# Optimization experiments

Hardware: AMD Instinct MI355X
Metric: run time of the kernel (lower is better)

Reference implementation:

```python
import jax, jax.numpy as jnp
import numpy as np


def setup_inputs() -> dict:
    key = jax.random.key(0)
    ks = jax.random.split(key, 5)
    B, S, D, U = 16, 4096, 256, 256
    scale = 1.0 / np.sqrt(D)
    return {
        "values": jax.random.normal(ks[0], (B, S, D), dtype=jnp.float32),
        "query": jax.random.normal(ks[1], (B, D), dtype=jnp.float32),
        "W1": jax.random.normal(ks[2], (D, U), dtype=jnp.float32) * scale,
        "b1": jnp.zeros((U,), dtype=jnp.float32),
        "W2": jax.random.normal(ks[3], (D, U), dtype=jnp.float32) * scale,
        "b2": jnp.zeros((U,), dtype=jnp.float32),
        "V": jax.random.normal(ks[4], (U, 1), dtype=jnp.float32) * (1.0 / np.sqrt(U)),
        "bV": jnp.zeros((1,), dtype=jnp.float32),
    }


def reference(values, query, W1, b1, W2, b2, V, bV):
    # values: [B, S, D], query: [B, D]
    proj_v = jnp.einsum("bsd,du->bsu", values, W1) + b1          # [B, S, U]
    proj_q = (query @ W2 + b2)[:, None, :]                        # [B, 1, U]
    score = jnp.tanh(proj_v + proj_q) @ V + bV                    # [B, S, 1]
    attention_weights = jax.nn.softmax(score, axis=1)             # [B, S, 1]
    context_vector = jnp.sum(attention_weights * values, axis=1)  # [B, D]
    return context_vector, attention_weights
```

## Files before the change

kernel.cpp:

```cpp
#include <hip/hip_runtime.h>
#include <hip/hip_bf16.h>

#define B 16
#define S 4096
#define D 256
#define U 256
#define ROWS 64
#define CHUNK 128
#define NCH (S / CHUNK)

typedef short short8 __attribute__((ext_vector_type(8)));
typedef float f32x4 __attribute__((ext_vector_type(4)));

__device__ __forceinline__ ushort f2bf(float f) {
    union { float f; uint u; } x{f};
    uint r = (x.u + 0x7fffu + ((x.u >> 16) & 1u)) >> 16;
    return (ushort)r;
}

__device__ __forceinline__ float fast_tanh(float x) {
    float e = __expf(2.0f * x);
    return 1.0f - 2.0f * __builtin_amdgcn_rcpf(e + 1.0f);
}

__global__ void ka_setup(const float* __restrict__ q, const float* __restrict__ W2,
                         const float* __restrict__ b2, const float* __restrict__ b1,
                         const float* __restrict__ W1, float* __restrict__ pqb,
                         ushort* __restrict__ W1p, float* __restrict__ ctx) {
    int bid = blockIdx.x, t = threadIdx.x;
    if (bid < 16) {
        int b = bid, u = t;
        const float* qb = q + b * D;
        float acc = b2[u] + b1[u];
#pragma unroll 8
        for (int d = 0; d < D; ++d)
            acc = fmaf(qb[d], W2[d * U + u], acc);
        pqb[b * U + u] = acc;
    } else if (bid < 24) {
        int kk = bid - 16;
        int l = t & 63, g = t >> 6;
        int colu0 = l & 15;
        int k0 = kk * 32 + (l >> 4) * 8;
#pragma unroll
        for (int i = 0; i < 4; ++i) {
            int nt = g * 4 + i;
            int colu = nt * 16 + colu0;
            ushort* dst = W1p + (((nt * 8) + kk) * 64 + l) * 8;
#pragma unroll
            for (int e = 0; e < 8; ++e) dst[e] = f2bf(W1[(k0 + e) * U + colu]);
        }
    } else {
        int i = (bid - 24) * 256 + t;
        ctx[i] = 0.f;
        ctx[i + 2048] = 0.f;
    }
}

__global__ void kb_scores(const float* __restrict__ values, const ushort* __restrict__ W1p,
                          const float* __restrict__ pqb, const float* __restrict__ V,
                          const float* __restrict__ bV, float* __restrict__ scores,
                          float* __restrict__ cstats) {
    __shared__ ushort Alds[ROWS * 256];
    __shared__ float red[4][ROWS];
    int b = blockIdx.x >> 6;
    int s0 = (blockIdx.x & 63) * ROWS;
    int t = threadIdx.x;
    int w = t >> 6, l = t & 63;
    char* lds = (char*)Alds;

    const float* src = values + ((size_t)(b * S + s0)) * D;
#pragma unroll
    for (int i = 0; i < 16; ++i) {
        int row = i * 4 + w;
        int col = l * 4;
        float4 v = *(const float4*)&src[row * 256 + col];
        ushort4 h;
        h.x = f2bf(v.x); h.y = f2bf(v.y); h.z = f2bf(v.z); h.w = f2bf(v.w);
        int byte = (row * 512 + col * 2) ^ ((row & 7) << 4);
        *(ushort4*)(lds + byte) = h;
    }
    __syncthreads();

    int lrow = l & 15, lk = l >> 4;
    f32x4 acc[4][4];
#pragma unroll
    for (int mt = 0; mt < 4; ++mt)
#pragma unroll
        for (int nt = 0; nt < 4; ++nt) acc[mt][nt] = (f32x4){0.f, 0.f, 0.f, 0.f};

    for (int kk = 0; kk < 8; ++kk) {
        short8 afr[4], bfr[4];
#pragma unroll
        for (int mt = 0; mt < 4; ++mt) {
            int row = mt * 16 + lrow;
            int byte = (row * 512 + kk * 64 + lk * 16) ^ ((row & 7) << 4);
            afr[mt] = *(const short8*)(lds + byte);
        }
#pragma unroll
        for (int nt = 0; nt < 4; ++nt) {
            int ntile = w * 4 + nt;
            bfr[nt] = *(const short8*)&W1p[(((ntile * 8) + kk) * 64 + l) * 8];
        }
#pragma unroll
        for (int mt = 0; mt < 4; ++mt)
#pragma unroll
            for (int nt = 0; nt < 4; ++nt)
                acc[mt][nt] = __builtin_amdgcn_mfma_f32_16x16x32_bf16(
                    afr[mt], bfr[nt], acc[mt][nt], 0, 0, 0);
    }

    float bb[4], vv[4];
#pragma unroll
    for (int nt = 0; nt < 4; ++nt) {
        int u = (w * 4 + nt) * 16 + lrow;
        bb[nt] = pqb[b * U + u];
        vv[nt] = V[u];
    }
#pragma unroll
    for (int mt = 0; mt < 4; ++mt) {
#pragma unroll
        for (int r = 0; r < 4; ++r) {
            float s = 0.f;
#pragma unroll
            for (int nt = 0; nt < 4; ++nt)
                s += fast_tanh(acc[mt][nt][r] + bb[nt]) * vv[nt];
            s += __shfl_xor(s, 1);
            s += __shfl_xor(s, 2);
            s += __shfl_xor(s, 4);
            s += __shfl_xor(s, 8);
            if (lrow == 0) red[w][mt * 16 + lk * 4 + r] = s;
        }
    }
    __syncthreads();
    if (t < ROWS) {
        float s = red[0][t] + red[1][t] + red[2][t] + red[3][t] + bV[0];
        scores[b * S + s0 + t] = s;
        float m = s;
#pragma unroll
        for (int off = 32; off; off >>= 1) m = fmaxf(m, __shfl_xor(m, off));
        float z = __expf(s - m);
#pragma unroll
        for (int off = 32; off; off >>= 1) z += __shfl_xor(z, off);
        if (t == 0) {
            cstats[2 * blockIdx.x] = m;
            cstats[2 * blockIdx.x + 1] = z;
        }
    }
}

__global__ void kc_ctx(const float* __restrict__ values, const float* __restrict__ scores,
                       const float* __restrict__ cstats, float* __restrict__ wout,
                       float* __restrict__ ctx) {
    __shared__ float wch[CHUNK];
    __shared__ float stats[2];
    __shared__ float part[4][D];
    int b = blockIdx.x / NCH;
    int c = blockIdx.x % NCH;
    int s0 = c * CHUNK;
    int t = threadIdx.x;

    if (t < 64) {
        float m = cstats[2 * (b * 64 + t)];
        float z = cstats[2 * (b * 64 + t) + 1];
        float M = m;
#pragma unroll
        for (int off = 32; off; off >>= 1) M = fmaxf(M, __shfl_xor(M, off));
        float zz = z * __expf(m - M);
#pragma unroll
        for (int off = 32; off; off >>= 1) zz += __shfl_xor(zz, off);
        if (t == 0) { stats[0] = M; stats[1] = zz; }
    }
    __syncthreads();
    float M = stats[0];
    float invZ = 1.0f / stats[1];

    if (t < CHUNK) {
        float w = __expf(scores[b * S + s0 + t] - M) * invZ;
        wch[t] = w;
        wout[b * S + s0 + t] = w;
    }
    __syncthreads();

    int sg = t >> 6, c4 = (t & 63) * 4;
    const float* vb = values + ((size_t)(b * S + s0 + sg * 32)) * D + c4;
    float4 acc = {0.f, 0.f, 0.f, 0.f};
#pragma unroll 4
    for (int s = 0; s < 32; ++s) {
        float4 v = *(const float4*)&vb[(size_t)s * D];
        float w = wch[sg * 32 + s];
        acc.x = fmaf(w, v.x, acc.x);
        acc.y = fmaf(w, v.y, acc.y);
        acc.z = fmaf(w, v.z, acc.z);
        acc.w = fmaf(w, v.w, acc.w);
    }
    *(float4*)&part[sg][c4] = acc;
    __syncthreads();

    float sum = part[0][t] + part[1][t] + part[2][t] + part[3][t];
    atomicAdd(&ctx[b * D + t], sum);
}

extern "C" void kernel_launch(void* const* d_in, const int* in_sizes, int n_in,
                              void* d_out, int out_size, void* d_ws, size_t ws_size,
                              hipStream_t stream) {
    const float* values = (const float*)d_in[0];
    const float* query  = (const float*)d_in[1];
    const float* W1     = (const float*)d_in[2];
    const float* b1     = (const float*)d_in[3];
    const float* W2     = (const float*)d_in[4];
    const float* b2     = (const float*)d_in[5];
    const float* V      = (const float*)d_in[6];
    const float* bV     = (const float*)d_in[7];

    float* out  = (float*)d_out;
    float* ctx  = out;
    float* wout = out + B * D;

    float* ws     = (float*)d_ws;
    float* pqb    = ws;
    float* scores = pqb + B * U;
    float* cstats = scores + B * S;
    ushort* W1p   = (ushort*)(cstats + 2048);

    ka_setup<<<32, 256, 0, stream>>>(query, W2, b2, b1, W1, pqb, W1p, ctx);
    kb_scores<<<B * (S / ROWS), 256, 0, stream>>>(values, W1p, pqb, V, bV, scores, cstats);
    kc_ctx<<<B * NCH, 256, 0, stream>>>(values, scores, cstats, wout, ctx);
}
```

Measured before the change: 49.66 us.

## Fuse context accumulation into score kernel using chunk-local softmax partials

```diff
diff --git a/kernel.cpp b/kernel.cpp
--- a/kernel.cpp
+++ b/kernel.cpp
@@ -6,8 +6,7 @@
 #define D 256
 #define U 256
 #define ROWS 64
-#define CHUNK 128
-#define NCH (S / CHUNK)
+#define NCHK (S / ROWS)
 
 typedef short short8 __attribute__((ext_vector_type(8)));
 typedef float f32x4 __attribute__((ext_vector_type(4)));
@@ -26,7 +25,7 @@
 __global__ void ka_setup(const float* __restrict__ q, const float* __restrict__ W2,
                          const float* __restrict__ b2, const float* __restrict__ b1,
                          const float* __restrict__ W1, float* __restrict__ pqb,
-                         ushort* __restrict__ W1p, float* __restrict__ ctx) {
+                         ushort* __restrict__ W1p) {
     int bid = blockIdx.x, t = threadIdx.x;
     if (bid < 16) {
         int b = bid, u = t;
@@ -36,7 +35,7 @@
         for (int d = 0; d < D; ++d)
             acc = fmaf(qb[d], W2[d * U + u], acc);
         pqb[b * U + u] = acc;
-    } else if (bid < 24) {
+    } else {
         int kk = bid - 16;
         int l = t & 63, g = t >> 6;
         int colu0 = l & 15;
@@ -49,19 +48,16 @@
 #pragma unroll
             for (int e = 0; e < 8; ++e) dst[e] = f2bf(W1[(k0 + e) * U + colu]);
         }
-    } else {
-        int i = (bid - 24) * 256 + t;
-        ctx[i] = 0.f;
-        ctx[i + 2048] = 0.f;
     }
 }
 
 __global__ void kb_scores(const float* __restrict__ values, const ushort* __restrict__ W1p,
                           const float* __restrict__ pqb, const float* __restrict__ V,
                           const float* __restrict__ bV, float* __restrict__ scores,
-                          float* __restrict__ cstats) {
+                          float* __restrict__ cstats, float* __restrict__ cpart) {
     __shared__ ushort Alds[ROWS * 256];
     __shared__ float red[4][ROWS];
+    __shared__ float wch[ROWS];
     int b = blockIdx.x >> 6;
     int s0 = (blockIdx.x & 63) * ROWS;
     int t = threadIdx.x;
@@ -138,7 +134,9 @@
         float m = s;
 #pragma unroll
         for (int off = 32; off; off >>= 1) m = fmaxf(m, __shfl_xor(m, off));
-        float z = __expf(s - m);
+        float z0 = __expf(s - m);
+        wch[t] = z0;
+        float z = z0;
 #pragma unroll
         for (int off = 32; off; off >>= 1) z += __shfl_xor(z, off);
         if (t == 0) {
@@ -146,58 +144,60 @@
             cstats[2 * blockIdx.x + 1] = z;
         }
     }
-}
-
-__global__ void kc_ctx(const float* __restrict__ values, const float* __restrict__ scores,
-                       const float* __restrict__ cstats, float* __restrict__ wout,
-                       float* __restrict__ ctx) {
-    __shared__ float wch[CHUNK];
+    __syncthreads();
+
+    const float* vsrc = values + ((size_t)(b * S + s0)) * D + t;
+    float cacc = 0.f;
+#pragma unroll 8
+    for (int r = 0; r < ROWS; ++r)
+        cacc = fmaf(wch[r], vsrc[(size_t)r * D], cacc);
+    cpart[(size_t)blockIdx.x * D + t] = cacc;
+}
+
+__global__ void kc_final(const float* __restrict__ scores, const float* __restrict__ cstats,
+                         const float* __restrict__ cpart, float* __restrict__ wout,
+                         float* __restrict__ ctx) {
+    __shared__ float scl[NCHK];
     __shared__ float stats[2];
-    __shared__ float part[4][D];
-    int b = blockIdx.x / NCH;
-    int c = blockIdx.x % NCH;
-    int s0 = c * CHUNK;
+    __shared__ float part[4][64];
+    int b = blockIdx.x >> 2, q = blockIdx.x & 3;
     int t = threadIdx.x;
 
     if (t < 64) {
-        float m = cstats[2 * (b * 64 + t)];
-        float z = cstats[2 * (b * 64 + t) + 1];
+        float m = cstats[2 * (b * NCHK + t)];
+        float z = cstats[2 * (b * NCHK + t) + 1];
         float M = m;
 #pragma unroll
         for (int off = 32; off; off >>= 1) M = fmaxf(M, __shfl_xor(M, off));
         float zz = z * __expf(m - M);
 #pragma unroll
         for (int off = 32; off; off >>= 1) zz += __shfl_xor(zz, off);
+        scl[t] = __expf(m - M);
         if (t == 0) { stats[0] = M; stats[1] = zz; }
     }
     __syncthreads();
     float M = stats[0];
     float invZ = 1.0f / stats[1];
 
-    if (t < CHUNK) {
-        float w = __expf(scores[b * S + s0 + t] - M) * invZ;
-        wch[t] = w;
-        wout[b * S + s0 + t] = w;
-    }
-    __syncthreads();
-
-    int sg = t >> 6, c4 = (t & 63) * 4;
-    const float* vb = values + ((size_t)(b * S + s0 + sg * 32)) * D + c4;
-    float4 acc = {0.f, 0.f, 0.f, 0.f};
-#pragma unroll 4
-    for (int s = 0; s < 32; ++s) {
-        float4 v = *(const float4*)&vb[(size_t)s * D];
-        float w = wch[sg * 32 + s];
-        acc.x = fmaf(w, v.x, acc.x);
-        acc.y = fmaf(w, v.y, acc.y);
-        acc.z = fmaf(w, v.z, acc.z);
-        acc.w = fmaf(w, v.w, acc.w);
-    }
-    *(float4*)&part[sg][c4] = acc;
-    __syncthreads();
-
-    float sum = part[0][t] + part[1][t] + part[2][t] + part[3][t];
-    atomicAdd(&ctx[b * D + t], sum);
+    int tq = t >> 6, dl = t & 63;
+    int d = q * 64 + dl;
+    float acc = 0.f;
+#pragma unroll
+    for (int i = 0; i < 16; ++i) {
+        int c = tq * 16 + i;
+        acc = fmaf(scl[c], cpart[(size_t)(b * NCHK + c) * D + d], acc);
+    }
+    part[tq][dl] = acc;
+
+#pragma unroll
+    for (int i = 0; i < 4; ++i) {
+        int s = q * 1024 + i * 256 + t;
+        wout[b * S + s] = __expf(scores[b * S + s] - M) * invZ;
+    }
+    __syncthreads();
+    if (t < 64)
+        ctx[b * D + q * 64 + t] =
+            (part[0][t] + part[1][t] + part[2][t] + part[3][t]) * invZ;
 }
 
 extern "C" void kernel_launch(void* const* d_in, const int* in_sizes, int n_in,
@@ -220,9 +220,10 @@
     float* pqb    = ws;
     float* scores = pqb + B * U;
     float* cstats = scores + B * S;
-    ushort* W1p   = (ushort*)(cstats + 2048);
-
-    ka_setup<<<32, 256, 0, stream>>>(query, W2, b2, b1, W1, pqb, W1p, ctx);
-    kb_scores<<<B * (S / ROWS), 256, 0, stream>>>(values, W1p, pqb, V, bV, scores, cstats);
-    kc_ctx<<<B * NCH, 256, 0, stream>>>(values, scores, cstats, wout, ctx);
-}
+    float* cpart  = cstats + 2048;
+    ushort* W1p   = (ushort*)(cpart + B * NCHK * D);
+
+    ka_setup<<<24, 256, 0, stream>>>(query, W2, b2, b1, W1, pqb, W1p);
+    kb_scores<<<B * NCHK, 256, 0, stream>>>(values, W1p, pqb, V, bV, scores, cstats, cpart);
+    kc_final<<<B * 4, 256, 0, stream>>>(scores, cstats, cpart, wout, ctx);
+}
```

Measured after the change: 46.75 us. -5.9%, faster.
